# Optimization experiments

Measured on AMD Instinct MI355X. Metric: run time of the kernel, lower is better.

Reference implementation:

```python
import jax, jax.numpy as jnp
import numpy as np

V, E, H, L, B, T = 32000, 512, 512, 2, 64, 256  # vocab, embed, per-layer hidden (1024//2), layers, batch, seq_len


def setup_inputs() -> dict:
    key = jax.random.key(0)
    ks = jax.random.split(key, 8)
    s = 1.0 / np.sqrt(H)  # PyTorch LSTM/Linear uniform init bound
    u = lambda k, shape: jax.random.uniform(k, shape, minval=-s, maxval=s, dtype=jnp.float32)
    return {
        "x": jax.random.randint(ks[0], (B, T), 0, V),
        "embedding": jax.random.normal(ks[1], (V, E), dtype=jnp.float32) * 0.02,
        "W_ih": u(ks[2], (L, 4 * H, E)),   # layer0 input=E, layer1 input=H (E==H here)
        "W_hh": u(ks[3], (L, 4 * H, H)),
        "b_ih": u(ks[4], (L, 4 * H)),
        "b_hh": u(ks[5], (L, 4 * H)),
        "W_fc": u(ks[6], (V, H)),
        "b_fc": u(ks[7], (V,)),
    }


def _lstm_stack(h, c, inp, W_ih, W_hh, b_ih, b_hh):
    # h, c: [L, B, H]; inp: [B, E]. PyTorch gate order: i, f, g, o.
    hs, cs = [], []
    for l in range(W_ih.shape[0]):
        gates = inp @ W_ih[l].T + b_ih[l] + h[l] @ W_hh[l].T + b_hh[l]  # [B, 4H]
        i, f, g, o = jnp.split(gates, 4, axis=-1)
        cn = jax.nn.sigmoid(f) * c[l] + jax.nn.sigmoid(i) * jnp.tanh(g)
        hn = jax.nn.sigmoid(o) * jnp.tanh(cn)
        hs.append(hn)
        cs.append(cn)
        inp = hn
    return jnp.stack(hs), jnp.stack(cs), inp


def reference(x, embedding, W_ih, W_hh, b_ih, b_hh, W_fc, b_fc):
    Bx, Tx = x.shape
    Hd = W_hh.shape[-1]
    Ly = W_ih.shape[0]
    Vx = embedding.shape[0]
    h0 = jnp.zeros((Ly, Bx, Hd), embedding.dtype)
    c0 = jnp.zeros((Ly, Bx, Hd), embedding.dtype)
    x0 = embedding[x[:, 0]]

    def step(carry, _):
        h, c, xt, _ = carry
        h, c, out = _lstm_stack(h, c, xt, W_ih, W_hh, b_ih, b_hh)
        logits = out @ W_fc.T + b_fc                      # [B, V]
        idx = jnp.argmax(logits, axis=1)                   # greedy decode
        xn = embedding[idx]                                # re-embed prediction
        return (h, c, xn, logits), None

    init = (h0, c0, x0, jnp.zeros((Bx, Vx), embedding.dtype))
    (h, c, xn, logits), _ = jax.lax.scan(step, init, None, length=Tx)
    return logits  # logits from the final decode step, [B, V]
```

## Files before the change

### kernel.cpp

```cpp
#include <hip/hip_runtime.h>
#include <stdint.h>

typedef unsigned long long u64;

#define Bq 64
#define Tq 256
#define Hq 512
#define Eq 512
#define Vq 32000

__device__ __forceinline__ float sigmoid_f(float x) { return 1.0f / (1.0f + expf(-x)); }

__device__ __forceinline__ unsigned f2sortable(float f) {
    unsigned u = __float_as_uint(f);
    return (u & 0x80000000u) ? ~u : (u | 0x80000000u);
}

__device__ __forceinline__ void gl_lds16(const float* g, float* l) {
    __builtin_amdgcn_global_load_lds(
        (const __attribute__((address_space(1))) void*)g,
        (__attribute__((address_space(3))) void*)l, 16, 0, 0);
}


#define DOT4(acc, a, wv) \
    acc = fmaf((a).w, (wv).w, fmaf((a).z, (wv).z, fmaf((a).y, (wv).y, fmaf((a).x, (wv).x, (acc)))))

__global__ __launch_bounds__(256) void lstm_layer_kernel(
    const float* __restrict__ emb,
    const int*   __restrict__ xcol,
    const u64*   __restrict__ amax_in,
    const float* __restrict__ inpT,
    const float* __restrict__ hprevT,
    float*       __restrict__ houtT,
    float*       __restrict__ cstate,
    const float* __restrict__ Wih,
    const float* __restrict__ Whh,
    const float* __restrict__ bih,
    const float* __restrict__ bhh,
    u64*         __restrict__ amax_reset,
    int t, int is_layer0)
{
    __shared__ float4 wlds[1024];
    const int h    = blockIdx.x;
    const int tid  = threadIdx.x;
    const int wave = __builtin_amdgcn_readfirstlane(tid >> 6);
    const int lane = tid & 63;

    if (amax_reset && blockIdx.x == 0 && wave == 3) amax_reset[lane] = 0;

    const float4* Wih4 = (const float4*)Wih;
    const float4* Whh4 = (const float4*)Whh;
    #pragma unroll
    for (int i = 0; i < 4; ++i) {
        int g   = i * 256 + tid;
        int s   = g >> 7;
        int off = g & 127;
        const float4* src = (s < 4) ? Wih4 : Whh4;
        wlds[g] = src[(size_t)((s & 3) * Hq + h) * 128 + off];
    }
    __syncthreads();

    const int part = wave >> 1;
    const int kq0  = (wave & 1) << 6;

    float acc0 = 0.f, acc1 = 0.f, acc2 = 0.f, acc3 = 0.f;

    if (part == 0 && is_layer0) {
        int row = (t == 0) ? xcol[lane * Tq] : (int)(~(unsigned)amax_in[lane]);
        const float4* a4 = (const float4*)(emb + (size_t)row * Eq);
        #pragma unroll 4
        for (int i = 0; i < 64; ++i) {
            float4 a = a4[kq0 + i];
            int kq = kq0 + i;
            float4 w0 = wlds[0 * 128 + kq];
            float4 w1 = wlds[1 * 128 + kq];
            float4 w2 = wlds[2 * 128 + kq];
            float4 w3 = wlds[3 * 128 + kq];
            DOT4(acc0, a, w0); DOT4(acc1, a, w1);
            DOT4(acc2, a, w2); DOT4(acc3, a, w3);
        }
    } else {
        const float4* a4 = (const float4*)(part ? hprevT : inpT);
        #pragma unroll 4
        for (int i = 0; i < 64; ++i) {
            int kq = kq0 + i;
            float4 a = a4[kq * 64 + lane];
            float4 w0 = wlds[(part * 4 + 0) * 128 + kq];
            float4 w1 = wlds[(part * 4 + 1) * 128 + kq];
            float4 w2 = wlds[(part * 4 + 2) * 128 + kq];
            float4 w3 = wlds[(part * 4 + 3) * 128 + kq];
            DOT4(acc0, a, w0); DOT4(acc1, a, w1);
            DOT4(acc2, a, w2); DOT4(acc3, a, w3);
        }
    }

    __shared__ float red[4][4][64];
    red[wave][0][lane] = acc0;
    red[wave][1][lane] = acc1;
    red[wave][2][lane] = acc2;
    red[wave][3][lane] = acc3;
    __syncthreads();

    if (wave == 0) {
        float gi = red[0][0][lane] + red[1][0][lane] + red[2][0][lane] + red[3][0][lane]
                 + bih[0 * Hq + h] + bhh[0 * Hq + h];
        float gf = red[0][1][lane] + red[1][1][lane] + red[2][1][lane] + red[3][1][lane]
                 + bih[1 * Hq + h] + bhh[1 * Hq + h];
        float gg = red[0][2][lane] + red[1][2][lane] + red[2][2][lane] + red[3][2][lane]
                 + bih[2 * Hq + h] + bhh[2 * Hq + h];
        float go = red[0][3][lane] + red[1][3][lane] + red[2][3][lane] + red[3][3][lane]
                 + bih[3 * Hq + h] + bhh[3 * Hq + h];
        float cold = cstate[h * 64 + lane];
        float cn = sigmoid_f(gf) * cold + sigmoid_f(gi) * tanhf(gg);
        float hn = sigmoid_f(go) * tanhf(cn);
        cstate[h * 64 + lane] = cn;
        houtT[(h >> 2) * 256 + lane * 4 + (h & 3)] = hn;
    }
}

__global__ __launch_bounds__(256) void fc_kernel(
    const float* __restrict__ hT,
    const float* __restrict__ Wfc,
    const float* __restrict__ bfc,
    float*       __restrict__ out,
    u64*         __restrict__ amax,
    int write_out)
{
    __shared__ float lds[2][8192];
    const int tid  = threadIdx.x;
    const int wave = __builtin_amdgcn_readfirstlane(tid >> 6);
    const int lane = tid & 63;
    const int rgrp = lane >> 3;
    const int bgrp = lane & 7;
    const int v0   = blockIdx.x * 64;

    float acc[8][8];
    #pragma unroll
    for (int j = 0; j < 8; ++j)
        #pragma unroll
        for (int i = 0; i < 8; ++i) acc[j][i] = 0.f;

#define STAGE_CHUNK(cc, dst)                                                  \
    {                                                                         \
        const int k0_ = (cc) * 64;                                            \
        _Pragma("unroll")                                                     \
        for (int it = 0; it < 4; ++it) {                                      \
            int g = it * 256 + tid;                                           \
            int r = g >> 4, sp = g & 15;                                      \
            int gk = k0_ + (((sp ^ (r >> 3)) & 15) << 2);                     \
            gl_lds16(Wfc + (size_t)(v0 + r) * 512 + gk,                       \
                     (dst) + it * 1024 + wave * 256);                         \
        }                                                                     \
        _Pragma("unroll")                                                     \
        for (int it = 0; it < 4; ++it) {                                      \
            int g = it * 256 + tid;                                           \
            int kqr = g >> 6, u = g & 63;                                     \
            int b = (u & 56) | ((u & 7) ^ (u >> 3));                          \
            gl_lds16(hT + (size_t)((cc) * 16 + kqr) * 256 + b * 4,            \
                     (dst) + 4096 + it * 1024 + wave * 256);                  \
        }                                                                     \
    }

    float* cur = lds[0];
    float* nxt = lds[1];

    STAGE_CHUNK(0, cur)
    __syncthreads();

    for (int c = 0; c < 8; ++c) {
        if (c < 7) STAGE_CHUNK(c + 1, nxt)

        #pragma unroll
        for (int kq = 0; kq < 4; ++kq) {
            const int sl = wave * 4 + kq;
            float4 wv[8], av[8];
            #pragma unroll
            for (int j = 0; j < 8; ++j)
                wv[j] = *(const float4*)(cur + (rgrp * 8 + j) * 64 + (((sl ^ rgrp) & 15) << 2));
            #pragma unroll
            for (int i = 0; i < 8; ++i)
                av[i] = *(const float4*)(cur + 4096 + sl * 256 + ((bgrp * 8 + (i ^ bgrp)) << 2));
            #pragma unroll
            for (int j = 0; j < 8; ++j)
                #pragma unroll
                for (int i = 0; i < 8; ++i)
                    DOT4(acc[j][i], av[i], wv[j]);
        }

        __syncthreads();
        float* tmp = cur; cur = nxt; nxt = tmp;
    }

    float* accbuf = lds[0];
    for (int w = 0; w < 4; ++w) {
        if (wave == w) {
            #pragma unroll
            for (int j = 0; j < 8; ++j) {
                float* p = accbuf + (rgrp * 8 + j) * 64 + bgrp * 8;
                if (w == 0) {
                    *(float4*)p       = make_float4(acc[j][0], acc[j][1], acc[j][2], acc[j][3]);
                    *(float4*)(p + 4) = make_float4(acc[j][4], acc[j][5], acc[j][6], acc[j][7]);
                } else {
                    float4 a0 = *(const float4*)p;
                    float4 a1 = *(const float4*)(p + 4);
                    a0.x += acc[j][0]; a0.y += acc[j][1]; a0.z += acc[j][2]; a0.w += acc[j][3];
                    a1.x += acc[j][4]; a1.y += acc[j][5]; a1.z += acc[j][6]; a1.w += acc[j][7];
                    *(float4*)p       = a0;
                    *(float4*)(p + 4) = a1;
                }
            }
        }
        __syncthreads();
    }

    const int b  = tid & 63;
    const int rq = wave;
    float best = -__builtin_huge_valf();
    int bi = 0;
    float lg[16];
    #pragma unroll
    for (int n = 0; n < 16; ++n) {
        int r = rq * 16 + n;
        float v = accbuf[r * 64 + b] + bfc[v0 + r];
        lg[n] = v;
        if (v > best) { best = v; bi = v0 + r; }
    }
    u64 pack = ((u64)f2sortable(best) << 32) | (u64)(~(unsigned)bi);

    u64* redm = (u64*)lds[1];
    redm[rq * 64 + b] = pack;
    __syncthreads();
    if (rq == 0) {
        u64 m  = redm[b];
        u64 m1 = redm[64 + b];  if (m1 > m) m = m1;
        u64 m2 = redm[128 + b]; if (m2 > m) m = m2;
        u64 m3 = redm[192 + b]; if (m3 > m) m = m3;
        atomicMax(&amax[b], m);
    }

    if (write_out) {
        #pragma unroll
        for (int n = 0; n < 16; ++n)
            out[(size_t)b * Vq + v0 + rq * 16 + n] = lg[n];
    }
}

extern "C" void kernel_launch(void* const* d_in, const int* in_sizes, int n_in,
                              void* d_out, int out_size, void* d_ws, size_t ws_size,
                              hipStream_t stream)
{
    const int*   x   = (const int*)d_in[0];
    const float* emb = (const float*)d_in[1];
    const float* Wih = (const float*)d_in[2];
    const float* Whh = (const float*)d_in[3];
    const float* bih = (const float*)d_in[4];
    const float* bhh = (const float*)d_in[5];
    const float* Wfc = (const float*)d_in[6];
    const float* bfc = (const float*)d_in[7];
    float* out = (float*)d_out;

    float* ws = (float*)d_ws;
    float* h0T[2] = { ws,          ws + 32768 };
    float* h1T[2] = { ws + 65536,  ws + 98304 };
    float* c0 = ws + 131072;
    float* c1 = ws + 163840;
    u64* amax = (u64*)(ws + 196608);

    hipMemsetAsync(d_ws, 0, 196608 * sizeof(float) + 64 * sizeof(u64), stream);

    const size_t WL = (size_t)4 * Hq * 512;
    for (int t = 0; t < Tq; ++t) {
        int rd = t & 1, wr = (t + 1) & 1;
        lstm_layer_kernel<<<512, 256, 0, stream>>>(
            emb, x, amax, nullptr, h0T[rd], h0T[wr], c0,
            Wih, Whh, bih, bhh,
            nullptr, t, 1);
        lstm_layer_kernel<<<512, 256, 0, stream>>>(
            emb, x, amax, h0T[wr], h1T[rd], h1T[wr], c1,
            Wih + WL, Whh + WL, bih + 4 * Hq, bhh + 4 * Hq,
            amax, t, 0);
        fc_kernel<<<500, 256, 0, stream>>>(
            h1T[wr], Wfc, bfc, out, amax, (t == Tq - 1) ? 1 : 0);
    }
}
```

Baseline: 21.19 ms.

## Fuse all timesteps into one persistent kernel with software grid barriers

```diff
diff --git a/kernel.cpp b/kernel.cpp
--- a/kernel.cpp
+++ b/kernel.cpp
@@ -8,6 +8,7 @@
 #define Hq 512
 #define Eq 512
 #define Vq 32000
+#define NBLK 256
 
 __device__ __forceinline__ float sigmoid_f(float x) { return 1.0f / (1.0f + expf(-x)); }
 
@@ -22,38 +23,46 @@
         (__attribute__((address_space(3))) void*)l, 16, 0, 0);
 }
 
-
 #define DOT4(acc, a, wv) \
     acc = fmaf((a).w, (wv).w, fmaf((a).z, (wv).z, fmaf((a).y, (wv).y, fmaf((a).x, (wv).x, (acc)))))
 
-__global__ __launch_bounds__(256) void lstm_layer_kernel(
-    const float* __restrict__ emb,
-    const int*   __restrict__ xcol,
-    const u64*   __restrict__ amax_in,
-    const float* __restrict__ inpT,
-    const float* __restrict__ hprevT,
-    float*       __restrict__ houtT,
-    float*       __restrict__ cstate,
-    const float* __restrict__ Wih,
-    const float* __restrict__ Whh,
-    const float* __restrict__ bih,
-    const float* __restrict__ bhh,
-    u64*         __restrict__ amax_reset,
+__device__ __forceinline__ void gbar(unsigned* cnt, unsigned* gen) {
+    __syncthreads();
+    if (threadIdx.x == 0) {
+        unsigned g = __hip_atomic_load(gen, __ATOMIC_RELAXED, __HIP_MEMORY_SCOPE_AGENT);
+        __threadfence();
+        unsigned a = __hip_atomic_fetch_add(cnt, 1u, __ATOMIC_ACQ_REL, __HIP_MEMORY_SCOPE_AGENT);
+        if (a == NBLK - 1u) {
+            __hip_atomic_store(cnt, 0u, __ATOMIC_RELAXED, __HIP_MEMORY_SCOPE_AGENT);
+            __hip_atomic_store(gen, g + 1u, __ATOMIC_RELEASE, __HIP_MEMORY_SCOPE_AGENT);
+        } else {
+            while (__hip_atomic_load(gen, __ATOMIC_ACQUIRE, __HIP_MEMORY_SCOPE_AGENT) == g)
+                __builtin_amdgcn_s_sleep(2);
+        }
+        __threadfence();
+    }
+    __syncthreads();
+}
+
+__device__ __forceinline__ void lstm_phase(
+    float* myl, int h, int wsub, int tsub,
+    const float* __restrict__ emb, const int* __restrict__ xcol,
+    const u64* __restrict__ amax_in,
+    const float* __restrict__ inpT, const float* __restrict__ hprevT,
+    float* __restrict__ houtT, float* __restrict__ cstate,
+    const float* __restrict__ Wih, const float* __restrict__ Whh,
+    const float* __restrict__ bih, const float* __restrict__ bhh,
     int t, int is_layer0)
 {
-    __shared__ float4 wlds[1024];
-    const int h    = blockIdx.x;
-    const int tid  = threadIdx.x;
-    const int wave = __builtin_amdgcn_readfirstlane(tid >> 6);
-    const int lane = tid & 63;
-
-    if (amax_reset && blockIdx.x == 0 && wave == 3) amax_reset[lane] = 0;
+    float4* wlds = (float4*)myl;
+    float*  red  = myl + 4096;
+    const int lane = tsub & 63;
 
     const float4* Wih4 = (const float4*)Wih;
     const float4* Whh4 = (const float4*)Whh;
     #pragma unroll
     for (int i = 0; i < 4; ++i) {
-        int g   = i * 256 + tid;
+        int g   = i * 256 + tsub;
         int s   = g >> 7;
         int off = g & 127;
         const float4* src = (s < 4) ? Wih4 : Whh4;
@@ -61,8 +70,8 @@
     }
     __syncthreads();
 
-    const int part = wave >> 1;
-    const int kq0  = (wave & 1) << 6;
+    const int part = wsub >> 1;
+    const int kq0  = (wsub & 1) << 6;
 
     float acc0 = 0.f, acc1 = 0.f, acc2 = 0.f, acc3 = 0.f;
 
@@ -95,21 +104,20 @@
         }
     }
 
-    __shared__ float red[4][4][64];
-    red[wave][0][lane] = acc0;
-    red[wave][1][lane] = acc1;
-    red[wave][2][lane] = acc2;
-    red[wave][3][lane] = acc3;
-    __syncthreads();
-
-    if (wave == 0) {
-        float gi = red[0][0][lane] + red[1][0][lane] + red[2][0][lane] + red[3][0][lane]
+    red[(wsub * 4 + 0) * 64 + lane] = acc0;
+    red[(wsub * 4 + 1) * 64 + lane] = acc1;
+    red[(wsub * 4 + 2) * 64 + lane] = acc2;
+    red[(wsub * 4 + 3) * 64 + lane] = acc3;
+    __syncthreads();
+
+    if (wsub == 0) {
+        float gi = red[(0*4+0)*64+lane] + red[(1*4+0)*64+lane] + red[(2*4+0)*64+lane] + red[(3*4+0)*64+lane]
                  + bih[0 * Hq + h] + bhh[0 * Hq + h];
-        float gf = red[0][1][lane] + red[1][1][lane] + red[2][1][lane] + red[3][1][lane]
+        float gf = red[(0*4+1)*64+lane] + red[(1*4+1)*64+lane] + red[(2*4+1)*64+lane] + red[(3*4+1)*64+lane]
                  + bih[1 * Hq + h] + bhh[1 * Hq + h];
-        float gg = red[0][2][lane] + red[1][2][lane] + red[2][2][lane] + red[3][2][lane]
+        float gg = red[(0*4+2)*64+lane] + red[(1*4+2)*64+lane] + red[(2*4+2)*64+lane] + red[(3*4+2)*64+lane]
                  + bih[2 * Hq + h] + bhh[2 * Hq + h];
-        float go = red[0][3][lane] + red[1][3][lane] + red[2][3][lane] + red[3][3][lane]
+        float go = red[(0*4+3)*64+lane] + red[(1*4+3)*64+lane] + red[(2*4+3)*64+lane] + red[(3*4+3)*64+lane]
                  + bih[3 * Hq + h] + bhh[3 * Hq + h];
         float cold = cstate[h * 64 + lane];
         float cn = sigmoid_f(gf) * cold + sigmoid_f(gi) * tanhf(gg);
@@ -119,21 +127,14 @@
     }
 }
 
-__global__ __launch_bounds__(256) void fc_kernel(
-    const float* __restrict__ hT,
-    const float* __restrict__ Wfc,
-    const float* __restrict__ bfc,
-    float*       __restrict__ out,
-    u64*         __restrict__ amax,
-    int write_out)
+__device__ __forceinline__ void fc_phase(
+    float* lds, int v0, int tid, int wave, int lane,
+    const float* __restrict__ hT, const float* __restrict__ Wfc,
+    const float* __restrict__ bfc, float* __restrict__ out,
+    u64* __restrict__ amax, int write_out)
 {
-    __shared__ float lds[2][8192];
-    const int tid  = threadIdx.x;
-    const int wave = __builtin_amdgcn_readfirstlane(tid >> 6);
-    const int lane = tid & 63;
     const int rgrp = lane >> 3;
     const int bgrp = lane & 7;
-    const int v0   = blockIdx.x * 64;
 
     float acc[8][8];
     #pragma unroll
@@ -145,25 +146,25 @@
     {                                                                         \
         const int k0_ = (cc) * 64;                                            \
         _Pragma("unroll")                                                     \
-        for (int it = 0; it < 4; ++it) {                                      \
-            int g = it * 256 + tid;                                           \
-            int r = g >> 4, sp = g & 15;                                      \
+        for (int it = 0; it < 2; ++it) {                                      \
+            int gf = it * 512 + tid;                                          \
+            int r = gf >> 4, sp = gf & 15;                                    \
             int gk = k0_ + (((sp ^ (r >> 3)) & 15) << 2);                     \
             gl_lds16(Wfc + (size_t)(v0 + r) * 512 + gk,                       \
-                     (dst) + it * 1024 + wave * 256);                         \
+                     (dst) + it * 2048 + wave * 256);                         \
         }                                                                     \
         _Pragma("unroll")                                                     \
-        for (int it = 0; it < 4; ++it) {                                      \
-            int g = it * 256 + tid;                                           \
-            int kqr = g >> 6, u = g & 63;                                     \
+        for (int it = 0; it < 2; ++it) {                                      \
+            int gf = it * 512 + tid;                                          \
+            int kqr = gf >> 6, u = gf & 63;                                   \
             int b = (u & 56) | ((u & 7) ^ (u >> 3));                          \
             gl_lds16(hT + (size_t)((cc) * 16 + kqr) * 256 + b * 4,            \
-                     (dst) + 4096 + it * 1024 + wave * 256);                  \
+                     (dst) + 4096 + it * 2048 + wave * 256);                  \
         }                                                                     \
     }
 
-    float* cur = lds[0];
-    float* nxt = lds[1];
+    float* cur = lds;
+    float* nxt = lds + 8192;
 
     STAGE_CHUNK(0, cur)
     __syncthreads();
@@ -172,8 +173,8 @@
         if (c < 7) STAGE_CHUNK(c + 1, nxt)
 
         #pragma unroll
-        for (int kq = 0; kq < 4; ++kq) {
-            const int sl = wave * 4 + kq;
+        for (int kq = 0; kq < 2; ++kq) {
+            const int sl = wave * 2 + kq;
             float4 wv[8], av[8];
             #pragma unroll
             for (int j = 0; j < 8; ++j)
@@ -191,58 +192,119 @@
         __syncthreads();
         float* tmp = cur; cur = nxt; nxt = tmp;
     }
-
-    float* accbuf = lds[0];
-    for (int w = 0; w < 4; ++w) {
-        if (wave == w) {
-            #pragma unroll
-            for (int j = 0; j < 8; ++j) {
-                float* p = accbuf + (rgrp * 8 + j) * 64 + bgrp * 8;
-                if (w == 0) {
-                    *(float4*)p       = make_float4(acc[j][0], acc[j][1], acc[j][2], acc[j][3]);
-                    *(float4*)(p + 4) = make_float4(acc[j][4], acc[j][5], acc[j][6], acc[j][7]);
-                } else {
-                    float4 a0 = *(const float4*)p;
-                    float4 a1 = *(const float4*)(p + 4);
-                    a0.x += acc[j][0]; a0.y += acc[j][1]; a0.z += acc[j][2]; a0.w += acc[j][3];
-                    a1.x += acc[j][4]; a1.y += acc[j][5]; a1.z += acc[j][6]; a1.w += acc[j][7];
-                    *(float4*)p       = a0;
-                    *(float4*)(p + 4) = a1;
-                }
-            }
-        }
-        __syncthreads();
-    }
-
-    const int b  = tid & 63;
-    const int rq = wave;
+#undef STAGE_CHUNK
+
+#define DUMP_ACC(buf)                                                         \
+    _Pragma("unroll")                                                         \
+    for (int j = 0; j < 8; ++j) {                                             \
+        float* p = (buf) + (rgrp * 8 + j) * 64 + bgrp * 8;                    \
+        *(float4*)p       = make_float4(acc[j][0], acc[j][1], acc[j][2], acc[j][3]); \
+        *(float4*)(p + 4) = make_float4(acc[j][4], acc[j][5], acc[j][6], acc[j][7]); \
+    }
+#define ADD_ACC(buf)                                                          \
+    _Pragma("unroll")                                                         \
+    for (int j = 0; j < 8; ++j) {                                             \
+        const float* p = (buf) + (rgrp * 8 + j) * 64 + bgrp * 8;              \
+        float4 a0 = *(const float4*)p;                                        \
+        float4 a1 = *(const float4*)(p + 4);                                  \
+        acc[j][0] += a0.x; acc[j][1] += a0.y; acc[j][2] += a0.z; acc[j][3] += a0.w; \
+        acc[j][4] += a1.x; acc[j][5] += a1.y; acc[j][6] += a1.z; acc[j][7] += a1.w; \
+    }
+
+    if (wave >= 4) DUMP_ACC(lds + (wave - 4) * 4096)
+    __syncthreads();
+    if (wave < 4)  ADD_ACC(lds + wave * 4096)
+    __syncthreads();
+    if (wave == 2 || wave == 3) DUMP_ACC(lds + (wave - 2) * 4096)
+    __syncthreads();
+    if (wave < 2)  ADD_ACC(lds + wave * 4096)
+    __syncthreads();
+    if (wave == 1) DUMP_ACC(lds)
+    __syncthreads();
+    if (wave == 0) { ADD_ACC(lds) }
+    __syncthreads();
+    if (wave == 0) DUMP_ACC(lds)
+    __syncthreads();
+#undef DUMP_ACC
+#undef ADD_ACC
+
+    const int b = lane;
     float best = -__builtin_huge_valf();
     int bi = 0;
-    float lg[16];
+    float lg[8];
     #pragma unroll
-    for (int n = 0; n < 16; ++n) {
-        int r = rq * 16 + n;
-        float v = accbuf[r * 64 + b] + bfc[v0 + r];
+    for (int n = 0; n < 8; ++n) {
+        int r = wave * 8 + n;
+        float v = lds[r * 64 + b] + bfc[v0 + r];
         lg[n] = v;
         if (v > best) { best = v; bi = v0 + r; }
     }
     u64 pack = ((u64)f2sortable(best) << 32) | (u64)(~(unsigned)bi);
 
-    u64* redm = (u64*)lds[1];
-    redm[rq * 64 + b] = pack;
-    __syncthreads();
-    if (rq == 0) {
-        u64 m  = redm[b];
-        u64 m1 = redm[64 + b];  if (m1 > m) m = m1;
-        u64 m2 = redm[128 + b]; if (m2 > m) m = m2;
-        u64 m3 = redm[192 + b]; if (m3 > m) m = m3;
+    u64* redm = (u64*)(lds + 8192);
+    redm[wave * 64 + b] = pack;
+    __syncthreads();
+    if (wave == 0) {
+        u64 m = redm[b];
+        #pragma unroll
+        for (int w = 1; w < 8; ++w) { u64 mw = redm[w * 64 + b]; if (mw > m) m = mw; }
         atomicMax(&amax[b], m);
     }
-
     if (write_out) {
         #pragma unroll
-        for (int n = 0; n < 16; ++n)
-            out[(size_t)b * Vq + v0 + rq * 16 + n] = lg[n];
+        for (int n = 0; n < 8; ++n)
+            out[(size_t)b * Vq + v0 + wave * 8 + n] = lg[n];
+    }
+}
+
+__global__ __launch_bounds__(512, 2) void fused_kernel(
+    const int* __restrict__ x, const float* __restrict__ emb,
+    const float* __restrict__ Wih, const float* __restrict__ Whh,
+    const float* __restrict__ bih, const float* __restrict__ bhh,
+    const float* __restrict__ Wfc, const float* __restrict__ bfc,
+    float* __restrict__ out, float* __restrict__ ws)
+{
+    __shared__ float lds[16384];
+    const int tid  = threadIdx.x;
+    const int wave = __builtin_amdgcn_readfirstlane(tid >> 6);
+    const int lane = tid & 63;
+    const int blk  = blockIdx.x;
+
+    float* h0T[2] = { ws,          ws + 32768 };
+    float* h1T[2] = { ws + 65536,  ws + 98304 };
+    float* c0 = ws + 131072;
+    float* c1 = ws + 163840;
+    u64* amax = (u64*)(ws + 196608);
+    unsigned* cnt = (unsigned*)(ws + 196800);
+    unsigned* gen = (unsigned*)(ws + 196832);
+
+    const int grpu = wave >> 2;
+    const int wsub = wave & 3;
+    const int tsub = tid & 255;
+    const int h    = blk + grpu * 256;
+    float* myl = lds + grpu * 5120;
+
+    const size_t WL = (size_t)4 * Hq * 512;
+
+    for (int t = 0; t < Tq; ++t) {
+        const int rd = t & 1, wr = rd ^ 1;
+
+        lstm_phase(myl, h, wsub, tsub, emb, x, amax,
+                   nullptr, h0T[rd], h0T[wr], c0,
+                   Wih, Whh, bih, bhh, t, 1);
+        gbar(cnt, gen);
+
+        if (blk == 0 && tid < 64) amax[tid] = 0;
+        lstm_phase(myl, h, wsub, tsub, emb, x, amax,
+                   h0T[wr], h1T[rd], h1T[wr], c1,
+                   Wih + WL, Whh + WL, bih + 4 * Hq, bhh + 4 * Hq, t, 0);
+        gbar(cnt, gen);
+
+        const int wo = (t == Tq - 1) ? 1 : 0;
+        fc_phase(lds, blk * 64, tid, wave, lane, h1T[wr], Wfc, bfc, out, amax, wo);
+        if (blk + 256 < 500)
+            fc_phase(lds, (blk + 256) * 64, tid, wave, lane, h1T[wr], Wfc, bfc, out, amax, wo);
+        gbar(cnt, gen);
     }
 }
 
@@ -258,29 +320,11 @@
     const float* bhh = (const float*)d_in[5];
     const float* Wfc = (const float*)d_in[6];
     const float* bfc = (const float*)d_in[7];
-    float* out = (float*)d_out;
-
-    float* ws = (float*)d_ws;
-    float* h0T[2] = { ws,          ws + 32768 };
-    float* h1T[2] = { ws + 65536,  ws + 98304 };
-    float* c0 = ws + 131072;
-    float* c1 = ws + 163840;
-    u64* amax = (u64*)(ws + 196608);
-
-    hipMemsetAsync(d_ws, 0, 196608 * sizeof(float) + 64 * sizeof(u64), stream);
-
-    const size_t WL = (size_t)4 * Hq * 512;
-    for (int t = 0; t < Tq; ++t) {
-        int rd = t & 1, wr = (t + 1) & 1;
-        lstm_layer_kernel<<<512, 256, 0, stream>>>(
-            emb, x, amax, nullptr, h0T[rd], h0T[wr], c0,
-            Wih, Whh, bih, bhh,
-            nullptr, t, 1);
-        lstm_layer_kernel<<<512, 256, 0, stream>>>(
-            emb, x, amax, h0T[wr], h1T[rd], h1T[wr], c1,
-            Wih + WL, Whh + WL, bih + 4 * Hq, bhh + 4 * Hq,
-            amax, t, 0);
-        fc_kernel<<<500, 256, 0, stream>>>(
-            h1T[wr], Wfc, bfc, out, amax, (t == Tq - 1) ? 1 : 0);
-    }
-}
+    float* outp = (float*)d_out;
+    float* wsf  = (float*)d_ws;
+
+    hipMemsetAsync(d_ws, 0, 196864 * sizeof(float), stream);
+
+    fused_kernel<<<NBLK, 512, 0, stream>>>(x, emb, Wih, Whh, bih, bhh,
+                                           Wfc, bfc, outp, wsf);
+}
```

Result: slower. 35.25 ms (+66.3%).

## Fuse all decode steps into one persistent kernel with hierarchical grid barrier

Applied to the files above, without the earlier changes.

```diff
diff --git a/kernel.cpp b/kernel.cpp
--- a/kernel.cpp
+++ b/kernel.cpp
@@ -8,6 +8,7 @@
 #define Hq 512
 #define Eq 512
 #define Vq 32000
+#define NBLK 512
 
 __device__ __forceinline__ float sigmoid_f(float x) { return 1.0f / (1.0f + expf(-x)); }
 
@@ -22,44 +23,46 @@
         (__attribute__((address_space(3))) void*)l, 16, 0, 0);
 }
 
-
 #define DOT4(acc, a, wv) \
     acc = fmaf((a).w, (wv).w, fmaf((a).z, (wv).z, fmaf((a).y, (wv).y, fmaf((a).x, (wv).x, (acc)))))
 
-__global__ __launch_bounds__(256) void lstm_layer_kernel(
-    const float* __restrict__ emb,
-    const int*   __restrict__ xcol,
-    const u64*   __restrict__ amax_in,
-    const float* __restrict__ inpT,
-    const float* __restrict__ hprevT,
-    float*       __restrict__ houtT,
-    float*       __restrict__ cstate,
-    const float* __restrict__ Wih,
-    const float* __restrict__ Whh,
-    const float* __restrict__ bih,
-    const float* __restrict__ bhh,
-    u64*         __restrict__ amax_reset,
+__device__ __forceinline__ void gbar(unsigned* bar, int blk, unsigned n) {
+    __syncthreads();
+    if (threadIdx.x == 0) {
+        __threadfence();
+        const int grp = blk >> 4;
+        unsigned prev = __hip_atomic_fetch_add(&bar[grp * 32], 1u,
+                            __ATOMIC_ACQ_REL, __HIP_MEMORY_SCOPE_AGENT);
+        if (prev == n * 16u - 1u) {
+            unsigned gp = __hip_atomic_fetch_add(&bar[1024], 1u,
+                            __ATOMIC_ACQ_REL, __HIP_MEMORY_SCOPE_AGENT);
+            if (gp == n * 32u - 1u)
+                __hip_atomic_store(&bar[1056], n, __ATOMIC_RELEASE,
+                                   __HIP_MEMORY_SCOPE_AGENT);
+        }
+        while (__hip_atomic_load(&bar[1056], __ATOMIC_ACQUIRE,
+                                 __HIP_MEMORY_SCOPE_AGENT) < n)
+            __builtin_amdgcn_s_sleep(1);
+        __threadfence();
+    }
+    __syncthreads();
+}
+
+
+__device__ __forceinline__ void lstm_phase(
+    float* lds, int layer, int h,
+    const float* __restrict__ emb, const int* __restrict__ xcol,
+    const u64* __restrict__ amax_in,
+    const float* __restrict__ inpT, const float* __restrict__ hprevT,
+    float* __restrict__ houtT, float* __restrict__ cstate,
+    const float* __restrict__ bih, const float* __restrict__ bhh,
     int t, int is_layer0)
 {
-    __shared__ float4 wlds[1024];
-    const int h    = blockIdx.x;
+    const float4* wlds = (const float4*)(lds + layer * 4096);
+    float* red = lds + 8192;
     const int tid  = threadIdx.x;
     const int wave = __builtin_amdgcn_readfirstlane(tid >> 6);
     const int lane = tid & 63;
-
-    if (amax_reset && blockIdx.x == 0 && wave == 3) amax_reset[lane] = 0;
-
-    const float4* Wih4 = (const float4*)Wih;
-    const float4* Whh4 = (const float4*)Whh;
-    #pragma unroll
-    for (int i = 0; i < 4; ++i) {
-        int g   = i * 256 + tid;
-        int s   = g >> 7;
-        int off = g & 127;
-        const float4* src = (s < 4) ? Wih4 : Whh4;
-        wlds[g] = src[(size_t)((s & 3) * Hq + h) * 128 + off];
-    }
-    __syncthreads();
 
     const int part = wave >> 1;
     const int kq0  = (wave & 1) << 6;
@@ -95,21 +98,20 @@
         }
     }
 
-    __shared__ float red[4][4][64];
-    red[wave][0][lane] = acc0;
-    red[wave][1][lane] = acc1;
-    red[wave][2][lane] = acc2;
-    red[wave][3][lane] = acc3;
+    red[(wave * 4 + 0) * 64 + lane] = acc0;
+    red[(wave * 4 + 1) * 64 + lane] = acc1;
+    red[(wave * 4 + 2) * 64 + lane] = acc2;
+    red[(wave * 4 + 3) * 64 + lane] = acc3;
     __syncthreads();
 
     if (wave == 0) {
-        float gi = red[0][0][lane] + red[1][0][lane] + red[2][0][lane] + red[3][0][lane]
+        float gi = red[(0*4+0)*64+lane] + red[(1*4+0)*64+lane] + red[(2*4+0)*64+lane] + red[(3*4+0)*64+lane]
                  + bih[0 * Hq + h] + bhh[0 * Hq + h];
-        float gf = red[0][1][lane] + red[1][1][lane] + red[2][1][lane] + red[3][1][lane]
+        float gf = red[(0*4+1)*64+lane] + red[(1*4+1)*64+lane] + red[(2*4+1)*64+lane] + red[(3*4+1)*64+lane]
                  + bih[1 * Hq + h] + bhh[1 * Hq + h];
-        float gg = red[0][2][lane] + red[1][2][lane] + red[2][2][lane] + red[3][2][lane]
+        float gg = red[(0*4+2)*64+lane] + red[(1*4+2)*64+lane] + red[(2*4+2)*64+lane] + red[(3*4+2)*64+lane]
                  + bih[2 * Hq + h] + bhh[2 * Hq + h];
-        float go = red[0][3][lane] + red[1][3][lane] + red[2][3][lane] + red[3][3][lane]
+        float go = red[(0*4+3)*64+lane] + red[(1*4+3)*64+lane] + red[(2*4+3)*64+lane] + red[(3*4+3)*64+lane]
                  + bih[3 * Hq + h] + bhh[3 * Hq + h];
         float cold = cstate[h * 64 + lane];
         float cn = sigmoid_f(gf) * cold + sigmoid_f(gi) * tanhf(gg);
@@ -119,21 +121,17 @@
     }
 }
 
-__global__ __launch_bounds__(256) void fc_kernel(
-    const float* __restrict__ hT,
-    const float* __restrict__ Wfc,
-    const float* __restrict__ bfc,
-    float*       __restrict__ out,
-    u64*         __restrict__ amax,
-    int write_out)
+__device__ __forceinline__ void fc_phase(
+    float* lds, int v0,
+    const float* __restrict__ hT, const float* __restrict__ Wfc,
+    const float* __restrict__ bfc, float* __restrict__ out,
+    u64* __restrict__ amax, int write_out)
 {
-    __shared__ float lds[2][8192];
     const int tid  = threadIdx.x;
     const int wave = __builtin_amdgcn_readfirstlane(tid >> 6);
     const int lane = tid & 63;
     const int rgrp = lane >> 3;
     const int bgrp = lane & 7;
-    const int v0   = blockIdx.x * 64;
 
     float acc[8][8];
     #pragma unroll
@@ -143,44 +141,45 @@
 
 #define STAGE_CHUNK(cc, dst)                                                  \
     {                                                                         \
-        const int k0_ = (cc) * 64;                                            \
         _Pragma("unroll")                                                     \
-        for (int it = 0; it < 4; ++it) {                                      \
+        for (int it = 0; it < 2; ++it) {                                      \
             int g = it * 256 + tid;                                           \
-            int r = g >> 4, sp = g & 15;                                      \
-            int gk = k0_ + (((sp ^ (r >> 3)) & 15) << 2);                     \
-            gl_lds16(Wfc + (size_t)(v0 + r) * 512 + gk,                       \
+            int r = g >> 3, sp = g & 7;                                       \
+            gl_lds16(Wfc + (size_t)(v0 + r) * 512 + (cc) * 32                 \
+                         + (((sp ^ (r >> 3)) & 7) << 2),                      \
                      (dst) + it * 1024 + wave * 256);                         \
         }                                                                     \
         _Pragma("unroll")                                                     \
-        for (int it = 0; it < 4; ++it) {                                      \
+        for (int it = 0; it < 2; ++it) {                                      \
             int g = it * 256 + tid;                                           \
             int kqr = g >> 6, u = g & 63;                                     \
             int b = (u & 56) | ((u & 7) ^ (u >> 3));                          \
-            gl_lds16(hT + (size_t)((cc) * 16 + kqr) * 256 + b * 4,            \
-                     (dst) + 4096 + it * 1024 + wave * 256);                  \
+            gl_lds16(hT + (size_t)((cc) * 8 + kqr) * 256 + b * 4,             \
+                     (dst) + 2048 + it * 1024 + wave * 256);                  \
         }                                                                     \
     }
 
-    float* cur = lds[0];
-    float* nxt = lds[1];
+    float* buf0 = lds + 9216;
+    float* buf1 = lds + 13312;
+    float* cur = buf0;
+    float* nxt = buf1;
 
     STAGE_CHUNK(0, cur)
     __syncthreads();
 
-    for (int c = 0; c < 8; ++c) {
-        if (c < 7) STAGE_CHUNK(c + 1, nxt)
+    for (int c = 0; c < 16; ++c) {
+        if (c < 15) STAGE_CHUNK(c + 1, nxt)
 
         #pragma unroll
-        for (int kq = 0; kq < 4; ++kq) {
-            const int sl = wave * 4 + kq;
+        for (int kq = 0; kq < 2; ++kq) {
+            const int sl = wave * 2 + kq;
             float4 wv[8], av[8];
             #pragma unroll
             for (int j = 0; j < 8; ++j)
-                wv[j] = *(const float4*)(cur + (rgrp * 8 + j) * 64 + (((sl ^ rgrp) & 15) << 2));
+                wv[j] = *(const float4*)(cur + (((rgrp * 8 + j) * 8 + ((sl ^ rgrp) & 7)) << 2));
             #pragma unroll
             for (int i = 0; i < 8; ++i)
-                av[i] = *(const float4*)(cur + 4096 + sl * 256 + ((bgrp * 8 + (i ^ bgrp)) << 2));
+                av[i] = *(const float4*)(cur + 2048 + sl * 256 + ((bgrp * 8 + (i ^ bgrp)) << 2));
             #pragma unroll
             for (int j = 0; j < 8; ++j)
                 #pragma unroll
@@ -191,8 +190,9 @@
         __syncthreads();
         float* tmp = cur; cur = nxt; nxt = tmp;
     }
-
-    float* accbuf = lds[0];
+#undef STAGE_CHUNK
+
+    float* accbuf = buf0;
     for (int w = 0; w < 4; ++w) {
         if (wave == w) {
             #pragma unroll
@@ -214,7 +214,7 @@
         __syncthreads();
     }
 
-    const int b  = tid & 63;
+    const int b  = lane;
     const int rq = wave;
     float best = -__builtin_huge_valf();
     int bi = 0;
@@ -228,7 +228,7 @@
     }
     u64 pack = ((u64)f2sortable(best) << 32) | (u64)(~(unsigned)bi);
 
-    u64* redm = (u64*)lds[1];
+    u64* redm = (u64*)(lds + 8192);
     redm[rq * 64 + b] = pack;
     __syncthreads();
     if (rq == 0) {
@@ -243,6 +243,64 @@
         #pragma unroll
         for (int n = 0; n < 16; ++n)
             out[(size_t)b * Vq + v0 + rq * 16 + n] = lg[n];
+    }
+}
+
+__global__ __launch_bounds__(256, 2) void fused_kernel(
+    const int* __restrict__ x, const float* __restrict__ emb,
+    const float* __restrict__ Wih, const float* __restrict__ Whh,
+    const float* __restrict__ bih, const float* __restrict__ bhh,
+    const float* __restrict__ Wfc, const float* __restrict__ bfc,
+    float* __restrict__ out, float* __restrict__ ws)
+{
+    __shared__ float lds[17408];
+    const int tid = threadIdx.x;
+    const int blk = blockIdx.x;
+    const int h   = blk;
+
+    float* h0T[2] = { ws,          ws + 32768 };
+    float* h1T[2] = { ws + 65536,  ws + 98304 };
+    float* c0 = ws + 131072;
+    float* c1 = ws + 163840;
+    u64* amax = (u64*)(ws + 196608);
+    unsigned* bar = (unsigned*)(ws + 196736);
+
+    const size_t WL = (size_t)4 * Hq * 512;
+    #pragma unroll
+    for (int l = 0; l < 2; ++l) {
+        const float4* Wih4 = (const float4*)(Wih + l * WL);
+        const float4* Whh4 = (const float4*)(Whh + l * WL);
+        float4* dstw = (float4*)(lds + l * 4096);
+        #pragma unroll
+        for (int i = 0; i < 4; ++i) {
+            int g   = i * 256 + tid;
+            int s   = g >> 7;
+            int off = g & 127;
+            const float4* src = (s < 4) ? Wih4 : Whh4;
+            dstw[g] = src[(size_t)((s & 3) * Hq + h) * 128 + off];
+        }
+    }
+    __syncthreads();
+
+    unsigned bn = 0;
+
+    for (int t = 0; t < Tq; ++t) {
+        const int rd = t & 1, wr = rd ^ 1;
+
+        lstm_phase(lds, 0, h, emb, x, amax,
+                   nullptr, h0T[rd], h0T[wr], c0, bih, bhh, t, 1);
+        gbar(bar, blk, ++bn);
+
+        if (blk == NBLK - 1 && tid < 64) amax[tid] = 0;
+        lstm_phase(lds, 1, h, emb, x, amax,
+                   h0T[wr], h1T[rd], h1T[wr], c1,
+                   bih + 4 * Hq, bhh + 4 * Hq, t, 0);
+        gbar(bar, blk, ++bn);
+
+        if (blk < 500)
+            fc_phase(lds, blk * 64, h1T[wr], Wfc, bfc, out, amax,
+                     (t == Tq - 1) ? 1 : 0);
+        gbar(bar, blk, ++bn);
     }
 }
 
@@ -258,29 +316,11 @@
     const float* bhh = (const float*)d_in[5];
     const float* Wfc = (const float*)d_in[6];
     const float* bfc = (const float*)d_in[7];
-    float* out = (float*)d_out;
-
-    float* ws = (float*)d_ws;
-    float* h0T[2] = { ws,          ws + 32768 };
-    float* h1T[2] = { ws + 65536,  ws + 98304 };
-    float* c0 = ws + 131072;
-    float* c1 = ws + 163840;
-    u64* amax = (u64*)(ws + 196608);
-
-    hipMemsetAsync(d_ws, 0, 196608 * sizeof(float) + 64 * sizeof(u64), stream);
-
-    const size_t WL = (size_t)4 * Hq * 512;
-    for (int t = 0; t < Tq; ++t) {
-        int rd = t & 1, wr = (t + 1) & 1;
-        lstm_layer_kernel<<<512, 256, 0, stream>>>(
-            emb, x, amax, nullptr, h0T[rd], h0T[wr], c0,
-            Wih, Whh, bih, bhh,
-            nullptr, t, 1);
-        lstm_layer_kernel<<<512, 256, 0, stream>>>(
-            emb, x, amax, h0T[wr], h1T[rd], h1T[wr], c1,
-            Wih + WL, Whh + WL, bih + 4 * Hq, bhh + 4 * Hq,
-            amax, t, 0);
-        fc_kernel<<<500, 256, 0, stream>>>(
-            h1T[wr], Wfc, bfc, out, amax, (t == Tq - 1) ? 1 : 0);
-    }
-}
+    float* outp = (float*)d_out;
+    float* wsf  = (float*)d_ws;
+
+    hipMemsetAsync(d_ws, 0, 197824 * sizeof(float), stream);
+
+    fused_kernel<<<NBLK, 256, 0, stream>>>(x, emb, Wih, Whh, bih, bhh,
+                                           Wfc, bfc, outp, wsf);
+}
```

Result: slower. 54.27 ms (+156.1%).
